# Optimization experiments

Measured on AMD Instinct MI355X. Metric: run time of the kernel, lower is better.

The kernel has to match this reference:

```python
import math
import jax, jax.numpy as jnp
import numpy as np

B, N, C = 2, 2048, 1024
H = 16
D = C // H  # 64
LN_EPS = 1e-5


def setup_inputs() -> dict:
    key = jax.random.key(0)
    ks = jax.random.split(key, 5)
    x = jax.random.normal(ks[0], (B, N, C), dtype=jnp.float32)
    w_qkv = jax.random.normal(ks[1], (C, 3 * C), dtype=jnp.float32) * 0.02
    w_proj = jax.random.normal(ks[2], (C, C), dtype=jnp.float32) * 0.02
    b_proj = jnp.zeros((C,), dtype=jnp.float32)
    ln_w = jnp.ones((D,), dtype=jnp.float32) + jax.random.normal(ks[3], (D,), dtype=jnp.float32) * 0.02
    ln_b = jax.random.normal(ks[4], (D,), dtype=jnp.float32) * 0.02
    return {"x": x, "w_qkv": w_qkv, "w_proj": w_proj, "b_proj": b_proj,
            "ln_w": ln_w, "ln_b": ln_b}


def _layernorm(t, w, b):
    mu = jnp.mean(t, axis=-1, keepdims=True)
    var = jnp.var(t, axis=-1, keepdims=True)
    return (t - mu) * jax.lax.rsqrt(var + LN_EPS) * w + b


def reference(x, w_qkv, w_proj, b_proj, ln_w, ln_b):
    b, n, c = x.shape
    h, d = H, c // H
    # QKV projection (no bias): [b,n,3c] -> [3,b,h,n,d]
    qkv = (x @ w_qkv).reshape(b, n, 3, h, d).transpose(2, 0, 3, 1, 4)
    q, k, v = qkv[0], qkv[1], qkv[2]
    # per-head LayerNorm on q and k (qk_norm)
    q = _layernorm(q, ln_w, ln_b)
    k = _layernorm(k, ln_w, ln_b)
    # NOTE: source multiplies q by sqrt(head_dim) (faithful to original)
    q = q * jnp.asarray(math.sqrt(d), dtype=q.dtype)
    scores = jnp.einsum('bhnd,bhmd->bhnm', q, k)  # [b,h,n,n]
    mask_value = -jnp.finfo(scores.dtype).max
    causal = jnp.tril(jnp.ones((n, n), dtype=bool))
    scores = jnp.where(causal, scores, mask_value)
    attn = jax.nn.softmax(scores, axis=-1)
    out = jnp.einsum('bhnm,bhmd->bhnd', attn, v)  # [b,h,n,d]
    out = out.transpose(0, 2, 1, 3).reshape(b, n, c)  # b n (h d)
    return out @ w_proj + b_proj
```

## Files before the change

### kernel.cpp

```cpp
#include <hip/hip_runtime.h>

#define LOG2E 1.4426950408889634f

typedef _Float16 f16x8_t __attribute__((ext_vector_type(8)));
typedef _Float16 f16x4_t __attribute__((ext_vector_type(4)));
typedef _Float16 f16x2_t __attribute__((ext_vector_type(2)));
typedef float    f32x4_t __attribute__((ext_vector_type(4)));

#define MFMA32(a, b, c) __builtin_amdgcn_mfma_f32_16x16x32_f16(a, b, c, 0, 0, 0)
#define MFMA16(a, b, c) __builtin_amdgcn_mfma_f32_16x16x16f16(a, b, c, 0, 0, 0)

__device__ __forceinline__ void async_copy16(void* lds, const void* g) {
    __builtin_amdgcn_global_load_lds(
        (const __attribute__((address_space(1))) unsigned char*)g,
        (__attribute__((address_space(3))) unsigned char*)lds, 16, 0, 0);
}

__global__ void prep_k(const float* __restrict__ x, _Float16* __restrict__ xh,
                       const float* __restrict__ wq, _Float16* __restrict__ wqT,
                       const float* __restrict__ wp, _Float16* __restrict__ wpT) {
    __shared__ _Float16 tl[64][65];
    const int bx = blockIdx.x, t = threadIdx.x;
    if (bx < 4096) {
        const int i = bx * 256 + t;
        float4 v = ((const float4*)x)[i];
        f16x4_t o = { (_Float16)v.x, (_Float16)v.y, (_Float16)v.z, (_Float16)v.w };
        ((f16x4_t*)xh)[i] = o;
        return;
    }
    const float* in; _Float16* out; int C, bxx, byy;
    if (bx < 4864) { const int id = bx - 4096; in = wq; out = wqT; C = 3072; bxx = id % 48; byy = id / 48; }
    else           { const int id = bx - 4864; in = wp; out = wpT; C = 1024; bxx = id % 16; byy = id / 16; }
    const int R = 1024;
    const int c = t & 63;
    const int r4 = t >> 6;
    const int r0 = byy * 64, c0 = bxx * 64;
#pragma unroll
    for (int i = 0; i < 16; ++i) {
        int r = r4 + i * 4;
        tl[c][r] = (_Float16)in[(size_t)(r0 + r) * C + c0 + c];
    }
    __syncthreads();
#pragma unroll
    for (int i = 0; i < 16; ++i) {
        int rr = r4 + i * 4;
        out[(size_t)(c0 + rr) * R + r0 + c] = tl[rr][c];
    }
}

template <typename OutT, bool BIAS, bool LNQK>
__global__ __launch_bounds__(256, 3)
void gemm_f16_k(const _Float16* __restrict__ A, const _Float16* __restrict__ BT,
                OutT* __restrict__ C, const float* __restrict__ bias,
                _Float16* __restrict__ VTg,
                const float* __restrict__ ln_w, const float* __restrict__ ln_b,
                int M, int N, int K) {
    __shared__ _Float16 As[2][128][32];
    __shared__ _Float16 Bs[2][128][32];
    const int tid = threadIdx.x;
    const int wid = tid >> 6, lane = tid & 63;
    const int qd = lane >> 4, ln = lane & 15;
    const int m0 = blockIdx.x * 128, n0 = blockIdx.y * 128;
    const int wm = (wid >> 1) * 64, wn = (wid & 1) * 64;

    f32x4_t acc[4][4] = {};

    const int srow = lane >> 2;
    const int skk  = (lane & 3) * 8;

    for (int k0 = 0; k0 < K; k0 += 64) {
        __syncthreads();
#pragma unroll
        for (int p = 0; p < 4; ++p) {
            const int seg = p * 4 + wid;
            const int s   = seg >> 3;
            const int rg  = seg & 7;
            const int row = rg * 16 + srow;
            const size_t goff = (size_t)row * K + k0 + s * 32 + skk;
            async_copy16(&As[0][0][0] + seg * 512, A  + (size_t)m0 * K + goff);
            async_copy16(&Bs[0][0][0] + seg * 512, BT + (size_t)n0 * K + goff);
        }
        __syncthreads();
#pragma unroll
        for (int s = 0; s < 2; ++s) {
            f16x8_t a[4], b[4];
#pragma unroll
            for (int i = 0; i < 4; ++i)
                a[i] = *(const f16x8_t*)&As[s][wm + i * 16 + ln][qd * 8];
#pragma unroll
            for (int j = 0; j < 4; ++j)
                b[j] = *(const f16x8_t*)&Bs[s][wn + j * 16 + ln][qd * 8];
#pragma unroll
            for (int i = 0; i < 4; ++i)
#pragma unroll
                for (int j = 0; j < 4; ++j)
                    acc[i][j] = MFMA32(a[i], b[j], acc[i][j]);
        }
    }

    if constexpr (LNQK) {
        if (n0 >= 2048) {
            __syncthreads();
            const int h2  = ((n0 - 2048) >> 6) + (wn >> 6);
            const int row0 = m0 + wm;
            const int bb  = row0 >> 11;
            const int tt  = (row0 & 2047) >> 6;
            const size_t obase = ((size_t)(bb * 16 + h2)) * 131072 + (size_t)tt * 4096;
            _Float16* tlw = &As[0][0][0] + wid * 1088;
#pragma unroll
            for (int j = 0; j < 4; ++j) {
#pragma unroll
                for (int i = 0; i < 4; ++i) {
                    f16x4_t v;
#pragma unroll
                    for (int r = 0; r < 4; ++r) v[r] = (_Float16)acc[i][j][r];
                    *(f16x4_t*)&tlw[ln * 68 + i * 16 + qd * 4] = v;
                }
#pragma unroll
                for (int e = 0; e < 2; ++e) {
                    const int ci = lane * 2 + e;
                    const int dl = ci >> 3, w2 = ci & 7;
                    const int pq = w2 ^ (dl & 7);
                    const int base = (pq >> 2) * 32 + (pq & 3) * 4;
                    f16x4_t v0 = *(const f16x4_t*)&tlw[dl * 68 + base];
                    f16x4_t v1 = *(const f16x4_t*)&tlw[dl * 68 + base + 16];
                    f16x8_t val = __builtin_shufflevector(v0, v1, 0, 1, 2, 3, 4, 5, 6, 7);
                    *(f16x8_t*)&VTg[obase + (size_t)((j * 16 + dl) * 8 + w2) * 8] = val;
                }
            }
            return;
        }
        {
            const float scale = (n0 < 1024) ? 8.0f * LOG2E : 1.0f;
            float lw[4], lb[4];
#pragma unroll
            for (int j = 0; j < 4; ++j) { lw[j] = ln_w[j * 16 + ln]; lb[j] = ln_b[j * 16 + ln]; }
#pragma unroll
            for (int i = 0; i < 4; ++i)
#pragma unroll
                for (int r = 0; r < 4; ++r) {
                    float s = acc[i][0][r] + acc[i][1][r] + acc[i][2][r] + acc[i][3][r];
                    s += __shfl_xor(s, 1); s += __shfl_xor(s, 2);
                    s += __shfl_xor(s, 4); s += __shfl_xor(s, 8);
                    const float mu = s * 0.015625f;
                    const float d0 = acc[i][0][r] - mu, d1 = acc[i][1][r] - mu;
                    const float d2 = acc[i][2][r] - mu, d3 = acc[i][3][r] - mu;
                    float v = d0 * d0 + d1 * d1 + d2 * d2 + d3 * d3;
                    v += __shfl_xor(v, 1); v += __shfl_xor(v, 2);
                    v += __shfl_xor(v, 4); v += __shfl_xor(v, 8);
                    const float rs = rsqrtf(v * 0.015625f + 1e-5f);
                    acc[i][0][r] = (d0 * rs * lw[0] + lb[0]) * scale;
                    acc[i][1][r] = (d1 * rs * lw[1] + lb[1]) * scale;
                    acc[i][2][r] = (d2 * rs * lw[2] + lb[2]) * scale;
                    acc[i][3][r] = (d3 * rs * lw[3] + lb[3]) * scale;
                }
        }
    }

#pragma unroll
    for (int i = 0; i < 4; ++i)
#pragma unroll
        for (int j = 0; j < 4; ++j) {
            const int col = n0 + wn + j * 16 + ln;
            const float bv = BIAS ? bias[col] : 0.0f;
#pragma unroll
            for (int r = 0; r < 4; ++r) {
                const int row = m0 + wm + i * 16 + qd * 4 + r;
                C[(size_t)row * N + col] = (OutT)(acc[i][j][r] + bv);
            }
        }
}

__global__ __launch_bounds__(256, 2)
void gemm_f16_m64_k(const _Float16* __restrict__ A, const _Float16* __restrict__ BT,
                    float* __restrict__ C, const float* __restrict__ bias,
                    int M, int N, int K) {
    __shared__ _Float16 As[2][64][32];
    __shared__ _Float16 Bs[2][128][32];
    const int tid = threadIdx.x;
    const int wid = tid >> 6, lane = tid & 63;
    const int qd = lane >> 4, ln = lane & 15;
    const int m0 = blockIdx.x * 64, n0 = blockIdx.y * 128;
    const int wn = wid * 32;

    f32x4_t acc[4][2] = {};
    const int srow = lane >> 2;
    const int skk  = (lane & 3) * 8;

    for (int k0 = 0; k0 < K; k0 += 64) {
        __syncthreads();
#pragma unroll
        for (int p = 0; p < 2; ++p) {
            const int seg = p * 4 + wid;
            const int hidx = seg * 512 + lane * 8;
            const int s_ = hidx >> 11;
            const int row = (hidx >> 5) & 63;
            const int kk = hidx & 31;
            async_copy16(&As[0][0][0] + seg * 512,
                         A + (size_t)(m0 + row) * K + k0 + s_ * 32 + kk);
        }
#pragma unroll
        for (int p = 0; p < 4; ++p) {
            const int seg = p * 4 + wid;
            const int s   = seg >> 3;
            const int rg  = seg & 7;
            const int row = rg * 16 + srow;
            async_copy16(&Bs[0][0][0] + seg * 512,
                         BT + (size_t)(n0 + row) * K + k0 + s * 32 + skk);
        }
        __syncthreads();
#pragma unroll
        for (int s = 0; s < 2; ++s) {
            f16x8_t a[4], b[2];
#pragma unroll
            for (int i = 0; i < 4; ++i)
                a[i] = *(const f16x8_t*)&As[s][i * 16 + ln][qd * 8];
#pragma unroll
            for (int j = 0; j < 2; ++j)
                b[j] = *(const f16x8_t*)&Bs[s][wn + j * 16 + ln][qd * 8];
#pragma unroll
            for (int i = 0; i < 4; ++i)
#pragma unroll
                for (int j = 0; j < 2; ++j)
                    acc[i][j] = MFMA32(a[i], b[j], acc[i][j]);
        }
    }
#pragma unroll
    for (int i = 0; i < 4; ++i)
#pragma unroll
        for (int j = 0; j < 2; ++j) {
            const int col = n0 + wn + j * 16 + ln;
            const float bv = bias[col];
#pragma unroll
            for (int r = 0; r < 4; ++r) {
                const int row = m0 + i * 16 + qd * 4 + r;
                C[(size_t)row * N + col] = acc[i][j][r] + bv;
            }
        }
}

__global__ __launch_bounds__(256, 3)
void attn_part_k(const _Float16* __restrict__ qkv, const _Float16* __restrict__ VTg,
                 _Float16* __restrict__ O, float* __restrict__ Op, float* __restrict__ ml) {
    __shared__ _Float16 Ks[2][2][64][32];
    __shared__ _Float16 VT[2][64][64];

    const int tid = threadIdx.x;
    const int wid = tid >> 6, lane = tid & 63;
    const int qd = lane >> 4, ln = lane & 15;
    const int bh = blockIdx.x;
    const int b = bh >> 4, h = bh & 15;
    const int y = blockIdx.y;
    int band, chunk, nst;
    if (y < 8)       { band = 8 + y;  chunk = 0; nst = 16; }
    else if (y < 16) { band = 23 - y; chunk = 1; nst = 2 * band - 14; }
    else             { band = y - 16; chunk = 0; nst = 2 * band + 2; }
    const size_t vtbase = (size_t)bh * 131072;
    const int qrow0 = band * 128 + wid * 32;
    const int kvbeg = chunk * 1024;

    f16x8_t qf[2][2];
#pragma unroll
    for (int qt = 0; qt < 2; ++qt)
#pragma unroll
        for (int s = 0; s < 2; ++s)
            qf[qt][s] = *(const f16x8_t*)&qkv[(size_t)(b * 2048 + qrow0 + qt * 16 + ln) * 3072
                                             + h * 64 + s * 32 + qd * 8];

    f32x4_t o[2][4] = {};
    f32x4_t ls[2] = {};
    float m[2] = { -3.0e38f, -3.0e38f };
    const f16x4_t ones = { (_Float16)1.0f, (_Float16)1.0f, (_Float16)1.0f, (_Float16)1.0f };

    auto stage = [&](int buf, int kv0) {
#pragma unroll
        for (int p = 0; p < 2; ++p) {
            const int seg = p * 4 + wid;
            const int hidx = seg * 512 + lane * 8;
            const int s_ = hidx >> 11;
            const int rrow = (hidx >> 5) & 63;
            const int kk = hidx & 31;
            async_copy16(&Ks[buf][0][0][0] + seg * 512,
                         qkv + (size_t)(b * 2048 + kv0 + rrow) * 3072 + 1024 + h * 64
                             + s_ * 32 + kk);
        }
#pragma unroll
        for (int p = 0; p < 2; ++p) {
            const int seg = p * 4 + wid;
            async_copy16(&VT[buf][0][0] + seg * 512,
                         VTg + vtbase + (size_t)kv0 * 64 + seg * 512 + lane * 8);
        }
    };

    stage(0, kvbeg);

    for (int st = 0; st < nst; ++st) {
        const int kv0 = kvbeg + st * 64;
        __syncthreads();
        if (st + 1 < nst) stage((st + 1) & 1, kv0 + 64);
        const int buf = st & 1;

        if (kv0 <= qrow0 + 31) {
            f32x4_t sc[2][4];
#pragma unroll
            for (int jt = 0; jt < 4; ++jt) {
                f16x8_t k0 = *(const f16x8_t*)&Ks[buf][0][jt * 16 + ln][qd * 8];
                f16x8_t k1 = *(const f16x8_t*)&Ks[buf][1][jt * 16 + ln][qd * 8];
#pragma unroll
                for (int qt = 0; qt < 2; ++qt) {
                    f32x4_t s = {};
                    s = MFMA32(k0, qf[qt][0], s);
                    s = MFMA32(k1, qf[qt][1], s);
                    sc[qt][jt] = s;
                }
            }
            f16x8_t vf8[4][2];
#pragma unroll
            for (int dt = 0; dt < 4; ++dt)
#pragma unroll
                for (int pp = 0; pp < 2; ++pp) {
                    const int w = (pp * 4 + qd) ^ (ln & 7);
                    vf8[dt][pp] = *(const f16x8_t*)&VT[buf][dt * 16 + ln][w * 8];
                }

#pragma unroll
            for (int qt = 0; qt < 2; ++qt) {
                if (kv0 + 63 > qrow0 + qt * 16) {
                    const int qq = qrow0 + qt * 16 + ln;
#pragma unroll
                    for (int c = 0; c < 4; ++c)
#pragma unroll
                        for (int r = 0; r < 4; ++r)
                            if (kv0 + c * 16 + qd * 4 + r > qq) sc[qt][c][r] = -3.0e38f;
                }
                float mx0 = fmaxf(fmaxf(fmaxf(sc[qt][0][0], sc[qt][1][0]), sc[qt][2][0]), sc[qt][3][0]);
                float mx1 = fmaxf(fmaxf(fmaxf(sc[qt][0][1], sc[qt][1][1]), sc[qt][2][1]), sc[qt][3][1]);
                float mx2 = fmaxf(fmaxf(fmaxf(sc[qt][0][2], sc[qt][1][2]), sc[qt][2][2]), sc[qt][3][2]);
                float mx3 = fmaxf(fmaxf(fmaxf(sc[qt][0][3], sc[qt][1][3]), sc[qt][2][3]), sc[qt][3][3]);
                float mx = fmaxf(fmaxf(fmaxf(mx0, mx1), mx2), mx3);
                mx = fmaxf(mx, __shfl_xor(mx, 16));
                mx = fmaxf(mx, __shfl_xor(mx, 32));
                if (!__all(mx <= m[qt] + 8.0f)) {
                    const float mn = fmaxf(m[qt], mx);
                    const float al = exp2f(m[qt] - mn);
#pragma unroll
                    for (int dt = 0; dt < 4; ++dt) o[qt][dt] *= al;
                    ls[qt][0] *= al;
                    m[qt] = mn;
                }
                f16x4_t pf[4];
#pragma unroll
                for (int c = 0; c < 4; ++c) {
                    float p0 = exp2f(sc[qt][c][0] - m[qt]);
                    float p1 = exp2f(sc[qt][c][1] - m[qt]);
                    float p2 = exp2f(sc[qt][c][2] - m[qt]);
                    float p3 = exp2f(sc[qt][c][3] - m[qt]);
                    f16x2_t a = __builtin_bit_cast(f16x2_t, __builtin_amdgcn_cvt_pkrtz(p0, p1));
                    f16x2_t bb = __builtin_bit_cast(f16x2_t, __builtin_amdgcn_cvt_pkrtz(p2, p3));
                    pf[c] = __builtin_shufflevector(a, bb, 0, 1, 2, 3);
                }
                __builtin_amdgcn_s_setprio(1);
#pragma unroll
                for (int c = 0; c < 4; ++c) ls[qt] = MFMA16(ones, pf[c], ls[qt]);
#pragma unroll
                for (int dt = 0; dt < 4; ++dt)
#pragma unroll
                    for (int pp = 0; pp < 2; ++pp) {
                        f16x4_t lo = __builtin_shufflevector(vf8[dt][pp], vf8[dt][pp], 0, 1, 2, 3);
                        f16x4_t hi = __builtin_shufflevector(vf8[dt][pp], vf8[dt][pp], 4, 5, 6, 7);
                        o[qt][dt] = MFMA16(lo, pf[pp * 2 + 0], o[qt][dt]);
                        o[qt][dt] = MFMA16(hi, pf[pp * 2 + 1], o[qt][dt]);
                    }
                __builtin_amdgcn_s_setprio(0);
            }
        }
    }

    if (band < 8) {
        const size_t base0 = ((size_t)(b * 2048 + qrow0 + ln)) * 1024 + h * 64 + qd * 4;
#pragma unroll
        for (int qt = 0; qt < 2; ++qt) {
            const float inv = 1.0f / ls[qt][0];
            const size_t base = base0 + (size_t)qt * 16 * 1024;
#pragma unroll
            for (int dt = 0; dt < 4; ++dt) {
                f16x4_t ov;
#pragma unroll
                for (int r = 0; r < 4; ++r) ov[r] = (_Float16)(o[qt][dt][r] * inv);
                *(f16x4_t*)&O[base + dt * 16] = ov;
            }
        }
    } else {
        const size_t pb = ((size_t)bh * 8 + (band - 8)) * 2 + chunk;
#pragma unroll
        for (int qt = 0; qt < 2; ++qt) {
            const int row = wid * 32 + qt * 16 + ln;
            float* op = Op + pb * 8192 + (size_t)row * 64 + qd * 4;
#pragma unroll
            for (int dt = 0; dt < 4; ++dt)
                *(f32x4_t*)&op[dt * 16] = o[qt][dt];
            if (qd == 0) {
                ml[pb * 256 + row * 2]     = m[qt];
                ml[pb * 256 + row * 2 + 1] = ls[qt][0];
            }
        }
    }
}

__global__ __launch_bounds__(256)
void attn_merge_k(const float* __restrict__ Op, const float* __restrict__ ml,
                  _Float16* __restrict__ O) {
    const int bh = blockIdx.x, bnd = blockIdx.y;
    const int b = bh >> 4, h = bh & 15;
    const int band = 8 + bnd;
    const size_t pb = ((size_t)bh * 8 + bnd) * 2;
    const int tid = threadIdx.x;
    const int row = tid >> 1;
    const int c32 = (tid & 1) * 32;
    const float m0 = ml[pb * 256 + row * 2],       l0 = ml[pb * 256 + row * 2 + 1];
    const float m1 = ml[(pb + 1) * 256 + row * 2], l1 = ml[(pb + 1) * 256 + row * 2 + 1];
    const float mm = fmaxf(m0, m1);
    const float a0 = exp2f(m0 - mm), a1 = exp2f(m1 - mm);
    const float inv = 1.0f / (l0 * a0 + l1 * a1);
    const float* p0 = Op + pb * 8192 + (size_t)row * 64 + c32;
    const float* p1 = p0 + 8192;
    _Float16* op = O + ((size_t)(b * 2048 + band * 128 + row)) * 1024 + h * 64 + c32;
#pragma unroll
    for (int g = 0; g < 8; ++g) {
        f32x4_t v0 = *(const f32x4_t*)&p0[g * 4];
        f32x4_t v1 = *(const f32x4_t*)&p1[g * 4];
        f16x4_t ov;
#pragma unroll
        for (int r = 0; r < 4; ++r)
            ov[r] = (_Float16)((v0[r] * a0 + v1[r] * a1) * inv);
        *(f16x4_t*)&op[g * 4] = ov;
    }
}

extern "C" void kernel_launch(void* const* d_in, const int* in_sizes, int n_in,
                              void* d_out, int out_size, void* d_ws, size_t ws_size,
                              hipStream_t stream) {
    const float* x      = (const float*)d_in[0];
    const float* w_qkv  = (const float*)d_in[1];
    const float* w_proj = (const float*)d_in[2];
    const float* b_proj = (const float*)d_in[3];
    const float* ln_w   = (const float*)d_in[4];
    const float* ln_b   = (const float*)d_in[5];
    float* out = (float*)d_out;

    char* w = (char*)d_ws;
    const size_t MB = 1024 * 1024;
    _Float16*  qkv    = (_Float16*)(w);
    _Float16*  xh     = (_Float16*)(w + 24 * MB);
    _Float16*  wqkvT  = (_Float16*)(w + 32 * MB);
    _Float16*  wprojT = (_Float16*)(w + 38 * MB);
    _Float16*  VTg    = (_Float16*)(w + 40 * MB);
    _Float16*  Ah     = (_Float16*)(w + 48 * MB);
    float*     Op     = (float*)(w + 56 * MB);
    float*     mlb    = (float*)(w + 72 * MB);

    prep_k<<<5120, 256, 0, stream>>>(x, xh, w_qkv, wqkvT, w_proj, wprojT);
    gemm_f16_k<_Float16, false, true><<<dim3(32, 24), 256, 0, stream>>>(
        xh, wqkvT, qkv, nullptr, VTg, ln_w, ln_b, 4096, 3072, 1024);
    attn_part_k<<<dim3(32, 24), 256, 0, stream>>>(qkv, VTg, Ah, Op, mlb);
    attn_merge_k<<<dim3(32, 8), 256, 0, stream>>>(Op, mlb, Ah);
    gemm_f16_m64_k<<<dim3(64, 8), 256, 0, stream>>>(Ah, wprojT, out, b_proj, 4096, 1024, 1024);
}
```

Measured before the change: 189.6 us.

## Load K and V fragments directly from global memory, dropping LDS staging

The attention kernel no longer double-buffers K and V^T tiles through shared memory with async global-to-LDS copies and per-step barriers. Each wave now loads its own K and V fragments straight from global memory into registers and skips KV tiles above the causal diagonal per wave. This removes the __syncthreads and LDS traffic, but each of the four waves now fetches the same K/V data separately, so the kernel relies on L1/L2 hits, and the loads are no longer prefetched ahead of compute.

```diff
diff --git a/kernel.cpp b/kernel.cpp
--- a/kernel.cpp
+++ b/kernel.cpp
@@ -242,9 +242,6 @@
 __global__ __launch_bounds__(256, 3)
 void attn_part_k(const _Float16* __restrict__ qkv, const _Float16* __restrict__ VTg,
                  _Float16* __restrict__ O, float* __restrict__ Op, float* __restrict__ ml) {
-    __shared__ _Float16 Ks[2][2][64][32];
-    __shared__ _Float16 VT[2][64][64];
-
     const int tid = threadIdx.x;
     const int wid = tid >> 6, lane = tid & 63;
     const int qd = lane >> 4, ln = lane & 15;
@@ -259,6 +256,9 @@
     const int qrow0 = band * 128 + wid * 32;
     const int kvbeg = chunk * 1024;
 
+    const _Float16* kbase = qkv + (size_t)b * 2048 * 3072 + 1024 + h * 64 + qd * 8;
+    const _Float16* vbase = VTg + vtbase + (size_t)ln * 64;
+
     f16x8_t qf[2][2];
 #pragma unroll
     for (int qt = 0; qt < 2; ++qt)
@@ -272,107 +272,86 @@
     float m[2] = { -3.0e38f, -3.0e38f };
     const f16x4_t ones = { (_Float16)1.0f, (_Float16)1.0f, (_Float16)1.0f, (_Float16)1.0f };
 
-    auto stage = [&](int buf, int kv0) {
-#pragma unroll
-        for (int p = 0; p < 2; ++p) {
-            const int seg = p * 4 + wid;
-            const int hidx = seg * 512 + lane * 8;
-            const int s_ = hidx >> 11;
-            const int rrow = (hidx >> 5) & 63;
-            const int kk = hidx & 31;
-            async_copy16(&Ks[buf][0][0][0] + seg * 512,
-                         qkv + (size_t)(b * 2048 + kv0 + rrow) * 3072 + 1024 + h * 64
-                             + s_ * 32 + kk);
-        }
-#pragma unroll
-        for (int p = 0; p < 2; ++p) {
-            const int seg = p * 4 + wid;
-            async_copy16(&VT[buf][0][0] + seg * 512,
-                         VTg + vtbase + (size_t)kv0 * 64 + seg * 512 + lane * 8);
-        }
-    };
-
-    stage(0, kvbeg);
-
     for (int st = 0; st < nst; ++st) {
         const int kv0 = kvbeg + st * 64;
-        __syncthreads();
-        if (st + 1 < nst) stage((st + 1) & 1, kv0 + 64);
-        const int buf = st & 1;
-
-        if (kv0 <= qrow0 + 31) {
-            f32x4_t sc[2][4];
-#pragma unroll
-            for (int jt = 0; jt < 4; ++jt) {
-                f16x8_t k0 = *(const f16x8_t*)&Ks[buf][0][jt * 16 + ln][qd * 8];
-                f16x8_t k1 = *(const f16x8_t*)&Ks[buf][1][jt * 16 + ln][qd * 8];
-#pragma unroll
-                for (int qt = 0; qt < 2; ++qt) {
-                    f32x4_t s = {};
-                    s = MFMA32(k0, qf[qt][0], s);
-                    s = MFMA32(k1, qf[qt][1], s);
-                    sc[qt][jt] = s;
+        if (kv0 > qrow0 + 31) continue;
+
+        f16x8_t kf[4][2];
+#pragma unroll
+        for (int jt = 0; jt < 4; ++jt) {
+            const _Float16* kr = kbase + (size_t)(kv0 + jt * 16 + ln) * 3072;
+            kf[jt][0] = *(const f16x8_t*)(kr);
+            kf[jt][1] = *(const f16x8_t*)(kr + 32);
+        }
+        f16x8_t vf8[4][2];
+#pragma unroll
+        for (int dt = 0; dt < 4; ++dt)
+#pragma unroll
+            for (int pp = 0; pp < 2; ++pp) {
+                const int w = (pp * 4 + qd) ^ (ln & 7);
+                vf8[dt][pp] = *(const f16x8_t*)&vbase[(size_t)kv0 * 64 + dt * 1024 + w * 8];
+            }
+
+        f32x4_t sc[2][4];
+#pragma unroll
+        for (int jt = 0; jt < 4; ++jt)
+#pragma unroll
+            for (int qt = 0; qt < 2; ++qt) {
+                f32x4_t s = {};
+                s = MFMA32(kf[jt][0], qf[qt][0], s);
+                s = MFMA32(kf[jt][1], qf[qt][1], s);
+                sc[qt][jt] = s;
+            }
+
+#pragma unroll
+        for (int qt = 0; qt < 2; ++qt) {
+            if (kv0 + 63 > qrow0 + qt * 16) {
+                const int qq = qrow0 + qt * 16 + ln;
+#pragma unroll
+                for (int c = 0; c < 4; ++c)
+#pragma unroll
+                    for (int r = 0; r < 4; ++r)
+                        if (kv0 + c * 16 + qd * 4 + r > qq) sc[qt][c][r] = -3.0e38f;
+            }
+            float mx0 = fmaxf(fmaxf(fmaxf(sc[qt][0][0], sc[qt][1][0]), sc[qt][2][0]), sc[qt][3][0]);
+            float mx1 = fmaxf(fmaxf(fmaxf(sc[qt][0][1], sc[qt][1][1]), sc[qt][2][1]), sc[qt][3][1]);
+            float mx2 = fmaxf(fmaxf(fmaxf(sc[qt][0][2], sc[qt][1][2]), sc[qt][2][2]), sc[qt][3][2]);
+            float mx3 = fmaxf(fmaxf(fmaxf(sc[qt][0][3], sc[qt][1][3]), sc[qt][2][3]), sc[qt][3][3]);
+            float mx = fmaxf(fmaxf(fmaxf(mx0, mx1), mx2), mx3);
+            mx = fmaxf(mx, __shfl_xor(mx, 16));
+            mx = fmaxf(mx, __shfl_xor(mx, 32));
+            if (!__all(mx <= m[qt] + 8.0f)) {
+                const float mn = fmaxf(m[qt], mx);
+                const float al = exp2f(m[qt] - mn);
+#pragma unroll
+                for (int dt = 0; dt < 4; ++dt) o[qt][dt] *= al;
+                ls[qt][0] *= al;
+                m[qt] = mn;
+            }
+            f16x4_t pf[4];
+#pragma unroll
+            for (int c = 0; c < 4; ++c) {
+                float p0 = exp2f(sc[qt][c][0] - m[qt]);
+                float p1 = exp2f(sc[qt][c][1] - m[qt]);
+                float p2 = exp2f(sc[qt][c][2] - m[qt]);
+                float p3 = exp2f(sc[qt][c][3] - m[qt]);
+                f16x2_t a = __builtin_bit_cast(f16x2_t, __builtin_amdgcn_cvt_pkrtz(p0, p1));
+                f16x2_t bb = __builtin_bit_cast(f16x2_t, __builtin_amdgcn_cvt_pkrtz(p2, p3));
+                pf[c] = __builtin_shufflevector(a, bb, 0, 1, 2, 3);
+            }
+            __builtin_amdgcn_s_setprio(1);
+#pragma unroll
+            for (int c = 0; c < 4; ++c) ls[qt] = MFMA16(ones, pf[c], ls[qt]);
+#pragma unroll
+            for (int dt = 0; dt < 4; ++dt)
+#pragma unroll
+                for (int pp = 0; pp < 2; ++pp) {
+                    f16x4_t lo = __builtin_shufflevector(vf8[dt][pp], vf8[dt][pp], 0, 1, 2, 3);
+                    f16x4_t hi = __builtin_shufflevector(vf8[dt][pp], vf8[dt][pp], 4, 5, 6, 7);
+                    o[qt][dt] = MFMA16(lo, pf[pp * 2 + 0], o[qt][dt]);
+                    o[qt][dt] = MFMA16(hi, pf[pp * 2 + 1], o[qt][dt]);
                 }
-            }
-            f16x8_t vf8[4][2];
-#pragma unroll
-            for (int dt = 0; dt < 4; ++dt)
-#pragma unroll
-                for (int pp = 0; pp < 2; ++pp) {
-                    const int w = (pp * 4 + qd) ^ (ln & 7);
-                    vf8[dt][pp] = *(const f16x8_t*)&VT[buf][dt * 16 + ln][w * 8];
-                }
-
-#pragma unroll
-            for (int qt = 0; qt < 2; ++qt) {
-                if (kv0 + 63 > qrow0 + qt * 16) {
-                    const int qq = qrow0 + qt * 16 + ln;
-#pragma unroll
-                    for (int c = 0; c < 4; ++c)
-#pragma unroll
-                        for (int r = 0; r < 4; ++r)
-                            if (kv0 + c * 16 + qd * 4 + r > qq) sc[qt][c][r] = -3.0e38f;
-                }
-                float mx0 = fmaxf(fmaxf(fmaxf(sc[qt][0][0], sc[qt][1][0]), sc[qt][2][0]), sc[qt][3][0]);
-                float mx1 = fmaxf(fmaxf(fmaxf(sc[qt][0][1], sc[qt][1][1]), sc[qt][2][1]), sc[qt][3][1]);
-                float mx2 = fmaxf(fmaxf(fmaxf(sc[qt][0][2], sc[qt][1][2]), sc[qt][2][2]), sc[qt][3][2]);
-                float mx3 = fmaxf(fmaxf(fmaxf(sc[qt][0][3], sc[qt][1][3]), sc[qt][2][3]), sc[qt][3][3]);
-                float mx = fmaxf(fmaxf(fmaxf(mx0, mx1), mx2), mx3);
-                mx = fmaxf(mx, __shfl_xor(mx, 16));
-                mx = fmaxf(mx, __shfl_xor(mx, 32));
-                if (!__all(mx <= m[qt] + 8.0f)) {
-                    const float mn = fmaxf(m[qt], mx);
-                    const float al = exp2f(m[qt] - mn);
-#pragma unroll
-                    for (int dt = 0; dt < 4; ++dt) o[qt][dt] *= al;
-                    ls[qt][0] *= al;
-                    m[qt] = mn;
-                }
-                f16x4_t pf[4];
-#pragma unroll
-                for (int c = 0; c < 4; ++c) {
-                    float p0 = exp2f(sc[qt][c][0] - m[qt]);
-                    float p1 = exp2f(sc[qt][c][1] - m[qt]);
-                    float p2 = exp2f(sc[qt][c][2] - m[qt]);
-                    float p3 = exp2f(sc[qt][c][3] - m[qt]);
-                    f16x2_t a = __builtin_bit_cast(f16x2_t, __builtin_amdgcn_cvt_pkrtz(p0, p1));
-                    f16x2_t bb = __builtin_bit_cast(f16x2_t, __builtin_amdgcn_cvt_pkrtz(p2, p3));
-                    pf[c] = __builtin_shufflevector(a, bb, 0, 1, 2, 3);
-                }
-                __builtin_amdgcn_s_setprio(1);
-#pragma unroll
-                for (int c = 0; c < 4; ++c) ls[qt] = MFMA16(ones, pf[c], ls[qt]);
-#pragma unroll
-                for (int dt = 0; dt < 4; ++dt)
-#pragma unroll
-                    for (int pp = 0; pp < 2; ++pp) {
-                        f16x4_t lo = __builtin_shufflevector(vf8[dt][pp], vf8[dt][pp], 0, 1, 2, 3);
-                        f16x4_t hi = __builtin_shufflevector(vf8[dt][pp], vf8[dt][pp], 4, 5, 6, 7);
-                        o[qt][dt] = MFMA16(lo, pf[pp * 2 + 0], o[qt][dt]);
-                        o[qt][dt] = MFMA16(hi, pf[pp * 2 + 1], o[qt][dt]);
-                    }
-                __builtin_amdgcn_s_setprio(0);
-            }
+            __builtin_amdgcn_s_setprio(0);
         }
     }
 
```

Result: slower. 196.3 us (+3.5%).
